# Kernel optimization log

Hardware: AMD Instinct MI355X
Metric: run time of the kernel (lower is better)

The kernel has to match this reference:

```python
import jax, jax.numpy as jnp
import numpy as np

B, S, H, T, F, L = 32, 512, 1024, 100, 512, 5  # batch, seq, hidden, num_topics, topic_hidden, n_langs
EPS = 1e-5


def _layernorm(x, g, b):
    mu = jnp.mean(x, axis=-1, keepdims=True)
    var = jnp.mean((x - mu) ** 2, axis=-1, keepdims=True)
    return (x - mu) * jax.lax.rsqrt(var + EPS) * g + b


def setup_inputs() -> dict:
    key = jax.random.key(0)
    ks = jax.random.split(key, 16)
    sc = 0.02
    return {
        "sequence_output": jax.random.normal(ks[0], (B, S, H), dtype=jnp.float32),
        "attention_mask": jnp.ones((B, S), dtype=jnp.float32),
        "language_ids": jax.random.randint(ks[1], (B,), 0, L, dtype=jnp.int32),
        "lda_features": jax.random.uniform(ks[2], (B, T), dtype=jnp.float32),
        # per-language adapter params (stacked over L)
        "W1": jax.random.normal(ks[3], (L, H, H), dtype=jnp.float32) * sc,
        "b1": jnp.zeros((L, H), dtype=jnp.float32),
        "g1": jnp.ones((L, H), dtype=jnp.float32),
        "beta1": jnp.zeros((L, H), dtype=jnp.float32),
        "W2": jax.random.normal(ks[4], (L, H, H), dtype=jnp.float32) * sc,
        "b2": jnp.zeros((L, H), dtype=jnp.float32),
        # topic fusion params
        "Wf": jax.random.normal(ks[5], (H + T, F), dtype=jnp.float32) * sc,
        "bf": jnp.zeros((F,), dtype=jnp.float32),
        "gf": jnp.ones((F,), dtype=jnp.float32),
        "betaf": jnp.zeros((F,), dtype=jnp.float32),
    }


def reference(sequence_output, attention_mask, language_ids, lda_features,
              W1, b1, g1, beta1, W2, b2, Wf, bf, gf, betaf):
    # Apply every language adapter to the full batch, then mask-accumulate
    # (faithful to the original anti-pattern).
    adapted = jnp.zeros_like(sequence_output)
    for lang in range(L):
        h = jnp.einsum("bsh,he->bse", sequence_output, W1[lang]) + b1[lang]
        h = jax.nn.relu(_layernorm(h, g1[lang], beta1[lang]))
        h = jnp.einsum("bsh,he->bse", h, W2[lang]) + b2[lang]
        lang_mask = (language_ids == lang).astype(sequence_output.dtype)[:, None, None]
        adapted = adapted + lang_mask * h
    # masked mean pool over sequence
    masked = adapted * attention_mask[:, :, None]
    pooled = masked.sum(axis=1) / attention_mask.sum(axis=1)[:, None]  # [B, H]
    combined = jnp.concatenate([pooled, lda_features], axis=-1)        # [B, H+T]
    fused = _layernorm(combined @ Wf + bf, gf, betaf)
    return jax.nn.relu(fused)  # dropout is identity in eval
```

## Files before the change

### kernel.cpp

```cpp
#include <hip/hip_runtime.h>
#include <hip/hip_bf16.h>
#include <stdint.h>

#define Bq 32
#define Sq 512
#define Hq 1024
#define Tq 100
#define Fq 512
#define Lq 5
#define EPSq 1e-5f

typedef float fx4 __attribute__((ext_vector_type(4)));
typedef __bf16 bfx8 __attribute__((ext_vector_type(8)));
typedef unsigned short u16x8 __attribute__((ext_vector_type(8)));
typedef unsigned short u16x4 __attribute__((ext_vector_type(4)));

static __device__ __forceinline__ unsigned short f2bf(float f) {
  unsigned int u = __builtin_bit_cast(unsigned int, f);
  return (unsigned short)((u + 0x7fffu + ((u >> 16) & 1u)) >> 16);
}
static __device__ __forceinline__ float bf2f(unsigned short s) {
  return __builtin_bit_cast(float, ((unsigned int)s) << 16);
}
static __device__ __forceinline__ unsigned short bfbits(float f) {
  __hip_bfloat16 h = __float2bfloat16(f);
  return __builtin_bit_cast(unsigned short, h);
}
static __device__ __forceinline__ u16x8 cvt8(float4 x0, float4 x1) {
  u16x8 r;
  r[0] = bfbits(x0.x); r[1] = bfbits(x0.y); r[2] = bfbits(x0.z); r[3] = bfbits(x0.w);
  r[4] = bfbits(x1.x); r[5] = bfbits(x1.y); r[6] = bfbits(x1.z); r[7] = bfbits(x1.w);
  return r;
}
static __device__ __forceinline__ void gl_lds16(const void* g, void* l) {
  __builtin_amdgcn_global_load_lds(
      (const __attribute__((address_space(1))) unsigned int*)(uintptr_t)g,
      (__attribute__((address_space(3))) unsigned int*)(uintptr_t)l,
      16, 0, 0);
}

__global__ void k_prep(const float* __restrict__ w1, unsigned short* __restrict__ w1t) {
  __shared__ float t[32][33];
  int blk = blockIdx.x;
  int l = blk >> 10; int rem = blk & 1023; int tr = rem >> 5; int tc = rem & 31;
  const float* src = w1 + (size_t)l * Hq * Hq;
  unsigned short* dst = w1t + (size_t)l * Hq * Hq;
  int tid = threadIdx.x;
  int tx = tid & 31, ty = tid >> 5;
#pragma unroll
  for (int p = 0; p < 4; p++)
    t[ty + 8 * p][tx] = src[(size_t)(tr * 32 + ty + 8 * p) * Hq + tc * 32 + tx];
  __syncthreads();
  int y0 = tid >> 3, xc = tid & 7;
  u16x4 o;
#pragma unroll
  for (int i = 0; i < 4; i++) o[i] = f2bf(t[4 * xc + i][y0]);
  *(u16x4*)(dst + (size_t)(tc * 32 + y0) * Hq + tr * 32 + 4 * xc) = o;
}

#define HS_ITER(HS, C0A, C0B, C1A, C1B, N0A, N0B, N1A, N1B)                          \
  do {                                                                               \
    int cur = (HS) & 3;                                                              \
    if ((HS) < 30)                                                                   \
      asm volatile("s_waitcnt vmcnt(8) lgkmcnt(0)\n\ts_barrier" ::: "memory");       \
    else                                                                             \
      asm volatile("s_waitcnt vmcnt(0) lgkmcnt(0)\n\ts_barrier" ::: "memory");       \
    if ((HS) <= 28) {                                                                \
      int ko = ((HS) + 3) * 32;                                                      \
      N0A = *(const float4*)(gAf0 + ko); N0B = *(const float4*)(gAf0 + ko + 4);      \
      N1A = *(const float4*)(gAf1 + ko); N1B = *(const float4*)(gAf1 + ko + 4);      \
      int slot = ((HS) + 3) & 3;                                                     \
      gl_lds16(gB[0] + ko, (char*)sB[slot] + dstOff[0]);                             \
      gl_lds16(gB[1] + ko, (char*)sB[slot] + dstOff[1]);                             \
    }                                                                                \
    __builtin_amdgcn_sched_barrier(0);  \
    const char* cA = (const char*)sA[cur];                                           \
    const char* cB = (const char*)sB[cur];                                           \
    bfx8 bfr[4], af[8];                                                              \
    _Pragma("unroll") for (int n = 0; n < 4; n++)                                    \
        bfr[n] = *(const bfx8*)(cB + bOff[n]);                                       \
    _Pragma("unroll") for (int m = 0; m < 8; m++)                                    \
        af[m] = *(const bfx8*)(cA + aOff[m]);                                        \
    __builtin_amdgcn_s_setprio(1);                                                   \
    _Pragma("unroll") for (int m = 0; m < 8; m++)                                    \
      _Pragma("unroll") for (int n = 0; n < 4; n++)                                  \
          acc[m][n] = __builtin_amdgcn_mfma_f32_16x16x32_bf16(af[m], bfr[n],         \
                                                              acc[m][n], 0, 0, 0);  \
    __builtin_amdgcn_s_setprio(0);                                                   \
    if ((HS) <= 29) {                                                                \
      int sa = ((HS) + 2) & 3;                                                       \
      *(u16x8*)((char*)sA[sa] + aW0) = cvt8(C0A, C0B);                               \
      *(u16x8*)((char*)sA[sa] + aW1) = cvt8(C1A, C1B);                               \
    }                                                                                \
  } while (0)

__global__ __launch_bounds__(512, 2) void k_gemm1(const float* __restrict__ seq,
                                                  const unsigned short* __restrict__ w1t,
                                                  const float* __restrict__ b1,
                                                  const int* __restrict__ lid,
                                                  unsigned short* __restrict__ h1bf) {
  __shared__ short sA[4][256 * 32];
  __shared__ short sB[4][256 * 32];
  int bid = blockIdx.x;
  int g = bid & 63; int tn = bid >> 6;
  int b = g >> 1; int tm = g & 1;
  int lang = lid[b];
  const float* Abf = seq + (size_t)b * Sq * Hq + (size_t)tm * 256 * Hq;
  const unsigned short* Bb = w1t + (size_t)lang * Hq * Hq + (size_t)tn * 256 * Hq;

  int tid = threadIdx.x;
  int lane = tid & 63; int wid = tid >> 6;
  int wr = wid >> 2, wc = wid & 3;
  int fr = lane & 15;
  int q = lane >> 4;
  int key = ((fr >> 1) & 7) << 4;

  const float* gAf0; const float* gAf1; int aW0, aW1;
  {
    int c0 = tid;       int R0 = c0 >> 2, q0 = c0 & 3; int y0 = R0 * 64 + q0 * 16;
    int c1 = tid + 512; int R1 = c1 >> 2, q1 = c1 & 3; int y1 = R1 * 64 + q1 * 16;
    aW0 = y0 ^ ((y0 >> 3) & 0x70);
    aW1 = y1 ^ ((y1 >> 3) & 0x70);
    gAf0 = Abf + (size_t)R0 * Hq + q0 * 8;
    gAf1 = Abf + (size_t)R1 * Hq + q1 * 8;
  }
  const unsigned short* gB[2]; int dstOff[2];
#pragma unroll
  for (int j = 0; j < 2; j++) {
    int p = (tid + j * 512) * 16;
    int l = p ^ ((p >> 3) & 0x70);
    int R = l >> 6, qa = (l >> 4) & 3;
    gB[j] = Bb + (size_t)R * Hq + qa * 8;
    dstOff[j] = p;
  }

  int aOff[8], bOff[4];
#pragma unroll
  for (int m = 0; m < 8; m++)
    aOff[m] = ((wr * 128 + m * 16 + fr) * 64 + q * 16) ^ key;
#pragma unroll
  for (int n = 0; n < 4; n++)
    bOff[n] = ((wc * 64 + n * 16 + fr) * 64 + q * 16) ^ key;

  fx4 acc[8][4];
#pragma unroll
  for (int m = 0; m < 8; m++)
#pragma unroll
    for (int n = 0; n < 4; n++) acc[m][n] = (fx4){0.f, 0.f, 0.f, 0.f};

  {
    float4 t0a = *(const float4*)(gAf0);      float4 t0b = *(const float4*)(gAf0 + 4);
    float4 t1a = *(const float4*)(gAf1);      float4 t1b = *(const float4*)(gAf1 + 4);
    *(u16x8*)((char*)sA[0] + aW0) = cvt8(t0a, t0b);
    *(u16x8*)((char*)sA[0] + aW1) = cvt8(t1a, t1b);
    t0a = *(const float4*)(gAf0 + 32); t0b = *(const float4*)(gAf0 + 36);
    t1a = *(const float4*)(gAf1 + 32); t1b = *(const float4*)(gAf1 + 36);
    *(u16x8*)((char*)sA[1] + aW0) = cvt8(t0a, t0b);
    *(u16x8*)((char*)sA[1] + aW1) = cvt8(t1a, t1b);
  }
  gl_lds16(gB[0],      (char*)sB[0] + dstOff[0]);
  gl_lds16(gB[1],      (char*)sB[0] + dstOff[1]);
  gl_lds16(gB[0] + 32, (char*)sB[1] + dstOff[0]);
  gl_lds16(gB[1] + 32, (char*)sB[1] + dstOff[1]);
  float4 x0a, x0b, x1a, x1b, y0a, y0b, y1a, y1b;
  x0a = *(const float4*)(gAf0 + 64); x0b = *(const float4*)(gAf0 + 68);
  x1a = *(const float4*)(gAf1 + 64); x1b = *(const float4*)(gAf1 + 68);
  gl_lds16(gB[0] + 64, (char*)sB[2] + dstOff[0]);
  gl_lds16(gB[1] + 64, (char*)sB[2] + dstOff[1]);

  for (int hs = 0; hs < 32; hs += 2) {
    HS_ITER(hs,     x0a, x0b, x1a, x1b, y0a, y0b, y1a, y1b);
    HS_ITER(hs + 1, y0a, y0b, y1a, y1b, x0a, x0b, x1a, x1b);
  }

  unsigned short* Cb = h1bf + (size_t)b * Sq * Hq;
  float bv[4];
#pragma unroll
  for (int n = 0; n < 4; n++)
    bv[n] = b1[lang * Hq + tn * 256 + wc * 64 + n * 16 + fr];
  int r0 = q * 4;
#pragma unroll
  for (int m = 0; m < 8; m++) {
#pragma unroll
    for (int n = 0; n < 4; n++) {
      int col = tn * 256 + wc * 64 + n * 16 + fr;
#pragma unroll
      for (int r = 0; r < 4; r++) {
        int row = tm * 256 + wr * 128 + m * 16 + r0 + r;
        Cb[(size_t)row * Hq + col] = f2bf(acc[m][n][r] + bv[n]);
      }
    }
  }
}

__global__ __launch_bounds__(256) void k_ln_pool(const unsigned short* __restrict__ h1bf,
                                                 const float* __restrict__ g1,
                                                 const float* __restrict__ be1,
                                                 const float* __restrict__ mask,
                                                 const int* __restrict__ lid,
                                                 float* __restrict__ partial) {
  __shared__ float sacc[4][1024];
  int blk = blockIdx.x; int b = blk >> 3; int ch = blk & 7;
  int tid = threadIdx.x; int lane = tid & 63; int w = tid >> 6;
  int lang = lid[b];
  int e0 = lane * 8;
  int e1 = 512 + lane * 8;

  const float4* gp = (const float4*)(g1 + (size_t)lang * Hq);
  const float4* bp = (const float4*)(be1 + (size_t)lang * Hq);
  float4 ga0 = gp[lane * 2], ga1 = gp[lane * 2 + 1];
  float4 gb0 = gp[128 + lane * 2], gb1 = gp[129 + lane * 2];
  float4 ba0 = bp[lane * 2], ba1 = bp[lane * 2 + 1];
  float4 bb0 = bp[128 + lane * 2], bb1 = bp[129 + lane * 2];
  float gA[8] = {ga0.x, ga0.y, ga0.z, ga0.w, ga1.x, ga1.y, ga1.z, ga1.w};
  float gB[8] = {gb0.x, gb0.y, gb0.z, gb0.w, gb1.x, gb1.y, gb1.z, gb1.w};
  float bA[8] = {ba0.x, ba0.y, ba0.z, ba0.w, ba1.x, ba1.y, ba1.z, ba1.w};
  float bB[8] = {bb0.x, bb0.y, bb0.z, bb0.w, bb1.x, bb1.y, bb1.z, bb1.w};

  float acc0[8] = {0, 0, 0, 0, 0, 0, 0, 0}, acc1[8] = {0, 0, 0, 0, 0, 0, 0, 0};

  for (int i = 0; i < 16; i++) {
    int s = ch * 64 + w * 16 + i;
    const unsigned short* rowp = h1bf + ((size_t)b * Sq + s) * Hq;
    u16x8 va = *(const u16x8*)(rowp + e0);
    u16x8 vb = *(const u16x8*)(rowp + e1);
    float xa[8], xb[8];
    float sum = 0.f, sq = 0.f;
#pragma unroll
    for (int j = 0; j < 8; j++) {
      xa[j] = bf2f(va[j]); sum += xa[j]; sq += xa[j] * xa[j];
      xb[j] = bf2f(vb[j]); sum += xb[j]; sq += xb[j] * xb[j];
    }
#pragma unroll
    for (int off = 1; off < 64; off <<= 1) {
      sum += __shfl_xor(sum, off, 64);
      sq += __shfl_xor(sq, off, 64);
    }
    float mu = sum * (1.f / Hq);
    float var = sq * (1.f / Hq) - mu * mu;
    float rstd = rsqrtf(var + EPSq);
    float mw = mask[b * Sq + s];
#pragma unroll
    for (int j = 0; j < 8; j++) {
      float y0 = fmaxf((xa[j] - mu) * rstd * gA[j] + bA[j], 0.f);
      float y1 = fmaxf((xb[j] - mu) * rstd * gB[j] + bB[j], 0.f);
      acc0[j] += mw * y0;
      acc1[j] += mw * y1;
    }
  }
#pragma unroll
  for (int j = 0; j < 8; j++) {
    sacc[w][e0 + j] = acc0[j];
    sacc[w][e1 + j] = acc1[j];
  }
  __syncthreads();
  int e = tid * 4;
#pragma unroll
  for (int j = 0; j < 4; j++)
    partial[(size_t)blk * Hq + e + j] =
        sacc[0][e + j] + sacc[1][e + j] + sacc[2][e + j] + sacc[3][e + j];
}

__global__ __launch_bounds__(256) void k_gemm2p(const float* __restrict__ partial,
                                                const float* __restrict__ mask,
                                                const float* __restrict__ w2,
                                                const int* __restrict__ lid,
                                                float* __restrict__ g2part) {
  __shared__ float pl[256];
  __shared__ float wsum[4];
  int blk = blockIdx.x;
  int b = blk >> 3; int ch = (blk >> 2) & 1; int ks = blk & 3;
  int tid = threadIdx.x;
  int lang = lid[b];
  float mv = mask[b * Sq + tid] + mask[b * Sq + 256 + tid];
#pragma unroll
  for (int off = 1; off < 64; off <<= 1) mv += __shfl_xor(mv, off, 64);
  if ((tid & 63) == 0) wsum[tid >> 6] = mv;
  __syncthreads();
  float inv = 1.0f / (wsum[0] + wsum[1] + wsum[2] + wsum[3]);
  float s = 0.f;
#pragma unroll
  for (int c = 0; c < 8; c++) s += partial[((size_t)(b * 8 + c)) * Hq + ks * 256 + tid];
  pl[tid] = s * inv;
  __syncthreads();
  int col = ch * 512 + tid * 2;
  const float* W = w2 + (size_t)lang * Hq * Hq + (size_t)ks * 256 * Hq + col;
  float a0 = 0.f, a1 = 0.f;
  for (int e0 = 0; e0 < 256; e0 += 8) {
    float2 w[8];
#pragma unroll
    for (int j = 0; j < 8; j++) w[j] = *(const float2*)(W + (size_t)(e0 + j) * Hq);
#pragma unroll
    for (int j = 0; j < 8; j++) { float c = pl[e0 + j]; a0 += c * w[j].x; a1 += c * w[j].y; }
  }
  float2* dst = (float2*)(g2part + ((size_t)(b * 4 + ks) * Hq) + col);
  *dst = make_float2(a0, a1);
}

__global__ __launch_bounds__(256) void k_fpart(const float* __restrict__ g2part,
                                               const float* __restrict__ b2,
                                               const int* __restrict__ lid,
                                               const float* __restrict__ lda,
                                               const float* __restrict__ wf,
                                               float* __restrict__ fpart) {
  __shared__ float sc[128];
  int blk = blockIdx.x;
  int b = blk / 9, ks = blk % 9;
  int tid = threadIdx.x;
  int klen = (ks < 8) ? 128 : 100;
  int kbase = (ks < 8) ? ks * 128 : Hq;
  if (ks < 8) {
    if (tid < 128) {
      int col = kbase + tid;
      float v = b2[lid[b] * Hq + col];
#pragma unroll
      for (int c = 0; c < 4; c++) v += g2part[((size_t)(b * 4 + c)) * Hq + col];
      sc[tid] = v;
    }
  } else if (tid < 100) {
    sc[tid] = lda[b * Tq + tid];
  }
  __syncthreads();
  const float* W = wf + (size_t)kbase * Fq + tid * 2;
  float a0 = 0.f, a1 = 0.f;
  int k0 = 0;
  for (; k0 + 8 <= klen; k0 += 8) {
    float2 w[8];
#pragma unroll
    for (int j = 0; j < 8; j++) w[j] = *(const float2*)(W + (size_t)(k0 + j) * Fq);
#pragma unroll
    for (int j = 0; j < 8; j++) { float c = sc[k0 + j]; a0 += c * w[j].x; a1 += c * w[j].y; }
  }
  for (; k0 < klen; k0++) {
    float2 w = *(const float2*)(W + (size_t)k0 * Fq);
    float c = sc[k0];
    a0 += c * w.x; a1 += c * w.y;
  }
  float2* dst = (float2*)(fpart + (size_t)blk * Fq + tid * 2);
  *dst = make_float2(a0, a1);
}

__global__ __launch_bounds__(512) void k_final2(const float* __restrict__ fpart,
                                                const float* __restrict__ bff,
                                                const float* __restrict__ gf,
                                                const float* __restrict__ betaf,
                                                float* __restrict__ out) {
  __shared__ float rsum[8], rsq[8];
  int b = blockIdx.x; int tid = threadIdx.x;
  float acc = bff[tid];
#pragma unroll
  for (int ks = 0; ks < 9; ks++) acc += fpart[((size_t)b * 9 + ks) * Fq + tid];
  float s = acc, q = acc * acc;
#pragma unroll
  for (int off = 1; off < 64; off <<= 1) {
    s += __shfl_xor(s, off, 64);
    q += __shfl_xor(q, off, 64);
  }
  int w = tid >> 6, lane = tid & 63;
  if (lane == 0) { rsum[w] = s; rsq[w] = q; }
  __syncthreads();
  float S = 0.f, Q = 0.f;
#pragma unroll
  for (int i = 0; i < 8; i++) { S += rsum[i]; Q += rsq[i]; }
  float mu = S * (1.f / Fq);
  float var = Q * (1.f / Fq) - mu * mu;
  float y = (acc - mu) * rsqrtf(var + EPSq) * gf[tid] + betaf[tid];
  y = fmaxf(y, 0.f);
  out[b * Fq + tid] = y;
}

extern "C" void kernel_launch(void* const* d_in, const int* in_sizes, int n_in,
                              void* d_out, int out_size, void* d_ws, size_t ws_size,
                              hipStream_t stream) {
  const float* seq = (const float*)d_in[0];
  const float* mask = (const float*)d_in[1];
  const int* lid = (const int*)d_in[2];
  const float* lda = (const float*)d_in[3];
  const float* W1 = (const float*)d_in[4];
  const float* b1 = (const float*)d_in[5];
  const float* g1 = (const float*)d_in[6];
  const float* be1 = (const float*)d_in[7];
  const float* W2 = (const float*)d_in[8];
  const float* b2 = (const float*)d_in[9];
  const float* Wf = (const float*)d_in[10];
  const float* bff = (const float*)d_in[11];
  const float* gf = (const float*)d_in[12];
  const float* betaf = (const float*)d_in[13];
  float* out = (float*)d_out;

  char* ws = (char*)d_ws;
  unsigned short* w1t = (unsigned short*)(ws);
  unsigned short* h1bf = (unsigned short*)(ws + 10485760);
  float* partial = (float*)(ws + 44040192);
  float* g2part = (float*)(ws + 45088768);
  float* fpart = (float*)(ws + 45613056);

  k_prep<<<5120, 256, 0, stream>>>(W1, w1t);
  k_gemm1<<<256, 512, 0, stream>>>(seq, w1t, b1, lid, h1bf);
  k_ln_pool<<<256, 256, 0, stream>>>(h1bf, g1, be1, mask, lid, partial);
  k_gemm2p<<<256, 256, 0, stream>>>(partial, mask, W2, lid, g2part);
  k_fpart<<<288, 256, 0, stream>>>(g2part, b2, lid, lda, Wf, fpart);
  k_final2<<<32, 512, 0, stream>>>(fpart, bff, gf, betaf, out);
}
```

Measured before the change: 92.90 us.

## Fuse topic-fusion GEMV and final layernorm into one tail kernel

Measured after the change: 109.1 us. 1.17x slower.

```diff
diff --git a/kernel.cpp b/kernel.cpp
--- a/kernel.cpp
+++ b/kernel.cpp
@@ -11,6 +11,7 @@
 #define EPSq 1e-5f
 
 typedef float fx4 __attribute__((ext_vector_type(4)));
+typedef float f32x4 __attribute__((ext_vector_type(4)));
 typedef __bf16 bfx8 __attribute__((ext_vector_type(8)));
 typedef unsigned short u16x8 __attribute__((ext_vector_type(8)));
 typedef unsigned short u16x4 __attribute__((ext_vector_type(4)));
@@ -26,11 +27,14 @@
   __hip_bfloat16 h = __float2bfloat16(f);
   return __builtin_bit_cast(unsigned short, h);
 }
-static __device__ __forceinline__ u16x8 cvt8(float4 x0, float4 x1) {
+static __device__ __forceinline__ u16x8 cvt8(f32x4 x0, f32x4 x1) {
   u16x8 r;
-  r[0] = bfbits(x0.x); r[1] = bfbits(x0.y); r[2] = bfbits(x0.z); r[3] = bfbits(x0.w);
-  r[4] = bfbits(x1.x); r[5] = bfbits(x1.y); r[6] = bfbits(x1.z); r[7] = bfbits(x1.w);
+  r[0] = bfbits(x0[0]); r[1] = bfbits(x0[1]); r[2] = bfbits(x0[2]); r[3] = bfbits(x0[3]);
+  r[4] = bfbits(x1[0]); r[5] = bfbits(x1[1]); r[6] = bfbits(x1[2]); r[7] = bfbits(x1[3]);
   return r;
+}
+static __device__ __forceinline__ f32x4 gload4(const float* p) {
+  return *(const __attribute__((address_space(1))) f32x4*)(uintptr_t)p;
 }
 static __device__ __forceinline__ void gl_lds16(const void* g, void* l) {
   __builtin_amdgcn_global_load_lds(
@@ -67,8 +71,8 @@
       asm volatile("s_waitcnt vmcnt(0) lgkmcnt(0)\n\ts_barrier" ::: "memory");       \
     if ((HS) <= 28) {                                                                \
       int ko = ((HS) + 3) * 32;                                                      \
-      N0A = *(const float4*)(gAf0 + ko); N0B = *(const float4*)(gAf0 + ko + 4);      \
-      N1A = *(const float4*)(gAf1 + ko); N1B = *(const float4*)(gAf1 + ko + 4);      \
+      N0A = gload4(gAf0 + ko); N0B = gload4(gAf0 + ko + 4);                          \
+      N1A = gload4(gAf1 + ko); N1B = gload4(gAf1 + ko + 4);                          \
       int slot = ((HS) + 3) & 3;                                                     \
       gl_lds16(gB[0] + ko, (char*)sB[slot] + dstOff[0]);                             \
       gl_lds16(gB[1] + ko, (char*)sB[slot] + dstOff[1]);                             \
@@ -149,12 +153,12 @@
     for (int n = 0; n < 4; n++) acc[m][n] = (fx4){0.f, 0.f, 0.f, 0.f};
 
   {
-    float4 t0a = *(const float4*)(gAf0);      float4 t0b = *(const float4*)(gAf0 + 4);
-    float4 t1a = *(const float4*)(gAf1);      float4 t1b = *(const float4*)(gAf1 + 4);
+    f32x4 t0a = gload4(gAf0);      f32x4 t0b = gload4(gAf0 + 4);
+    f32x4 t1a = gload4(gAf1);      f32x4 t1b = gload4(gAf1 + 4);
     *(u16x8*)((char*)sA[0] + aW0) = cvt8(t0a, t0b);
     *(u16x8*)((char*)sA[0] + aW1) = cvt8(t1a, t1b);
-    t0a = *(const float4*)(gAf0 + 32); t0b = *(const float4*)(gAf0 + 36);
-    t1a = *(const float4*)(gAf1 + 32); t1b = *(const float4*)(gAf1 + 36);
+    t0a = gload4(gAf0 + 32); t0b = gload4(gAf0 + 36);
+    t1a = gload4(gAf1 + 32); t1b = gload4(gAf1 + 36);
     *(u16x8*)((char*)sA[1] + aW0) = cvt8(t0a, t0b);
     *(u16x8*)((char*)sA[1] + aW1) = cvt8(t1a, t1b);
   }
@@ -162,9 +166,9 @@
   gl_lds16(gB[1],      (char*)sB[0] + dstOff[1]);
   gl_lds16(gB[0] + 32, (char*)sB[1] + dstOff[0]);
   gl_lds16(gB[1] + 32, (char*)sB[1] + dstOff[1]);
-  float4 x0a, x0b, x1a, x1b, y0a, y0b, y1a, y1b;
-  x0a = *(const float4*)(gAf0 + 64); x0b = *(const float4*)(gAf0 + 68);
-  x1a = *(const float4*)(gAf1 + 64); x1b = *(const float4*)(gAf1 + 68);
+  f32x4 x0a, x0b, x1a, x1b, y0a, y0b, y1a, y1b;
+  x0a = gload4(gAf0 + 64); x0b = gload4(gAf0 + 68);
+  x1a = gload4(gAf1 + 64); x1b = gload4(gAf1 + 68);
   gl_lds16(gB[0] + 64, (char*)sB[2] + dstOff[0]);
   gl_lds16(gB[1] + 64, (char*)sB[2] + dstOff[1]);
 
@@ -297,67 +301,48 @@
   *dst = make_float2(a0, a1);
 }
 
-__global__ __launch_bounds__(256) void k_fpart(const float* __restrict__ g2part,
-                                               const float* __restrict__ b2,
-                                               const int* __restrict__ lid,
-                                               const float* __restrict__ lda,
-                                               const float* __restrict__ wf,
-                                               float* __restrict__ fpart) {
-  __shared__ float sc[128];
-  int blk = blockIdx.x;
-  int b = blk / 9, ks = blk % 9;
-  int tid = threadIdx.x;
-  int klen = (ks < 8) ? 128 : 100;
-  int kbase = (ks < 8) ? ks * 128 : Hq;
-  if (ks < 8) {
-    if (tid < 128) {
-      int col = kbase + tid;
-      float v = b2[lid[b] * Hq + col];
-#pragma unroll
-      for (int c = 0; c < 4; c++) v += g2part[((size_t)(b * 4 + c)) * Hq + col];
-      sc[tid] = v;
-    }
-  } else if (tid < 100) {
-    sc[tid] = lda[b * Tq + tid];
-  }
-  __syncthreads();
-  const float* W = wf + (size_t)kbase * Fq + tid * 2;
-  float a0 = 0.f, a1 = 0.f;
-  int k0 = 0;
-  for (; k0 + 8 <= klen; k0 += 8) {
-    float2 w[8];
-#pragma unroll
-    for (int j = 0; j < 8; j++) w[j] = *(const float2*)(W + (size_t)(k0 + j) * Fq);
-#pragma unroll
-    for (int j = 0; j < 8; j++) { float c = sc[k0 + j]; a0 += c * w[j].x; a1 += c * w[j].y; }
-  }
-  for (; k0 < klen; k0++) {
-    float2 w = *(const float2*)(W + (size_t)k0 * Fq);
-    float c = sc[k0];
-    a0 += c * w.x; a1 += c * w.y;
-  }
-  float2* dst = (float2*)(fpart + (size_t)blk * Fq + tid * 2);
-  *dst = make_float2(a0, a1);
-}
-
-__global__ __launch_bounds__(512) void k_final2(const float* __restrict__ fpart,
-                                                const float* __restrict__ bff,
-                                                const float* __restrict__ gf,
-                                                const float* __restrict__ betaf,
-                                                float* __restrict__ out) {
+__global__ __launch_bounds__(512) void k_tail(const float* __restrict__ g2part,
+                                              const float* __restrict__ b2,
+                                              const int* __restrict__ lid,
+                                              const float* __restrict__ lda,
+                                              const float* __restrict__ wf,
+                                              const float* __restrict__ bff,
+                                              const float* __restrict__ gf,
+                                              const float* __restrict__ betaf,
+                                              float* __restrict__ out) {
+  __shared__ float sc[Hq + Tq];
   __shared__ float rsum[8], rsq[8];
   int b = blockIdx.x; int tid = threadIdx.x;
+  int lang = lid[b];
+#pragma unroll
+  for (int h = 0; h < 2; h++) {
+    int c = tid + h * 512;
+    float v = b2[lang * Hq + c];
+#pragma unroll
+    for (int k = 0; k < 4; k++) v += g2part[((size_t)(b * 4 + k)) * Hq + c];
+    sc[c] = v;
+  }
+  if (tid < Tq) sc[Hq + tid] = lda[b * Tq + tid];
+  __syncthreads();
   float acc = bff[tid];
-#pragma unroll
-  for (int ks = 0; ks < 9; ks++) acc += fpart[((size_t)b * 9 + ks) * Fq + tid];
+  const float* W = wf + tid;
+  int k0 = 0;
+  for (; k0 + 8 <= Hq + Tq; k0 += 8) {
+    float w[8];
+#pragma unroll
+    for (int j = 0; j < 8; j++) w[j] = W[(size_t)(k0 + j) * Fq];
+#pragma unroll
+    for (int j = 0; j < 8; j++) acc += sc[k0 + j] * w[j];
+  }
+  for (; k0 < Hq + Tq; k0++) acc += sc[k0] * W[(size_t)k0 * Fq];
   float s = acc, q = acc * acc;
 #pragma unroll
   for (int off = 1; off < 64; off <<= 1) {
     s += __shfl_xor(s, off, 64);
     q += __shfl_xor(q, off, 64);
   }
-  int w = tid >> 6, lane = tid & 63;
-  if (lane == 0) { rsum[w] = s; rsq[w] = q; }
+  int w8 = tid >> 6, lane = tid & 63;
+  if (lane == 0) { rsum[w8] = s; rsq[w8] = q; }
   __syncthreads();
   float S = 0.f, Q = 0.f;
 #pragma unroll
@@ -365,8 +350,7 @@
   float mu = S * (1.f / Fq);
   float var = Q * (1.f / Fq) - mu * mu;
   float y = (acc - mu) * rsqrtf(var + EPSq) * gf[tid] + betaf[tid];
-  y = fmaxf(y, 0.f);
-  out[b * Fq + tid] = y;
+  out[b * Fq + tid] = fmaxf(y, 0.f);
 }
 
 extern "C" void kernel_launch(void* const* d_in, const int* in_sizes, int n_in,
@@ -393,12 +377,10 @@
   unsigned short* h1bf = (unsigned short*)(ws + 10485760);
   float* partial = (float*)(ws + 44040192);
   float* g2part = (float*)(ws + 45088768);
-  float* fpart = (float*)(ws + 45613056);
 
   k_prep<<<5120, 256, 0, stream>>>(W1, w1t);
   k_gemm1<<<256, 512, 0, stream>>>(seq, w1t, b1, lid, h1bf);
   k_ln_pool<<<256, 256, 0, stream>>>(h1bf, g1, be1, mask, lid, partial);
   k_gemm2p<<<256, 256, 0, stream>>>(partial, mask, W2, lid, g2part);
-  k_fpart<<<288, 256, 0, stream>>>(g2part, b2, lid, lda, Wf, fpart);
-  k_final2<<<32, 512, 0, stream>>>(fpart, bff, gf, betaf, out);
-}
+  k_tail<<<32, 512, 0, stream>>>(g2part, b2, lid, lda, Wf, bff, gf, betaf, out);
+}
```
